# Performance work log

Measured on AMD Instinct MI355X. Metric: run time of the kernel, lower is better.

## Reference

```python
import jax, jax.numpy as jnp
import numpy as np

STRIDE = 32
NUM_CLASSES = 20
CONF_THRESH = 0.01
NMS_THRESH = 0.5
INPUT_H, INPUT_W = 1024, 1024
EPS = 1e-28


def make_grid(h, w):
    hs, ws = h // STRIDE, w // STRIDE
    gy, gx = jnp.meshgrid(jnp.arange(hs), jnp.arange(ws), indexing='ij')
    # [1, hs*ws, 2] (x, y) cell coordinates
    return jnp.stack([gx, gy], axis=-1).reshape(1, hs * ws, 2).astype(jnp.float32)


def decode_boxes(txtytwth, grid):
    # txtytwth: [B, N, 4] -> [xmin, ymin, xmax, ymax] in pixels
    cxy = (jax.nn.sigmoid(txtytwth[..., :2]) + grid) * STRIDE
    wh = jnp.exp(txtytwth[..., 2:])
    return jnp.concatenate([cxy - wh * 0.5, cxy + wh * 0.5], axis=-1)


def pairwise_iou(boxes):
    # boxes: [N, 4]; faithful to source: area without +1, w/h clamped to 1e-28
    x1, y1, x2, y2 = boxes[:, 0], boxes[:, 1], boxes[:, 2], boxes[:, 3]
    areas = (x2 - x1) * (y2 - y1)
    xx1 = jnp.maximum(x1[:, None], x1[None, :])
    yy1 = jnp.maximum(y1[:, None], y1[None, :])
    xx2 = jnp.minimum(x2[:, None], x2[None, :])
    yy2 = jnp.minimum(y2[:, None], y2[None, :])
    w = jnp.maximum(EPS, xx2 - xx1)
    h = jnp.maximum(EPS, yy2 - yy1)
    inter = w * h
    return inter / (areas[:, None] + areas[None, :] - inter)


def nms_single(boxes, scores, valid):
    # greedy NMS, fixed-shape: returns keep mask [N] in original order
    n = boxes.shape[0]
    order = jnp.argsort(-scores)
    b = boxes[order]
    v = valid[order]
    iou = pairwise_iou(b)  # [N, N]
    idx = jnp.arange(n)

    def body(i, keep):
        sup = keep[i] & (iou[i] > NMS_THRESH) & (idx > i)
        return keep & jnp.logical_not(sup)

    keep_sorted = jax.lax.fori_loop(0, n, body, v)
    return jnp.zeros(n, dtype=bool).at[order].set(keep_sorted)


def setup_inputs() -> dict:
    key = jax.random.key(0)
    k1, k2, k3 = jax.random.split(key, 3)
    feat = jax.random.normal(k1, (64, 512, 32, 32), dtype=jnp.float32)
    w_pred = jax.random.normal(k2, (25, 512), dtype=jnp.float32) * 0.05
    b_pred = jax.random.normal(k3, (25,), dtype=jnp.float32) * 0.05
    return {"feat": feat, "w_pred": w_pred, "b_pred": b_pred}


def reference(feat, w_pred, b_pred):
    B, C, hs, ws = feat.shape
    N = hs * ws
    # 1x1 conv head: [B, 25, hs, ws] -> [B, N, 25]
    pred = jnp.einsum('bchw,oc->bhwo', feat, w_pred) + b_pred
    pred = pred.reshape(B, N, 1 + NUM_CLASSES + 4)

    conf = jax.nn.sigmoid(pred[..., :1])                      # [B, N, 1]
    cls = jax.nn.softmax(pred[..., 1:1 + NUM_CLASSES], -1)    # [B, N, 20]
    boxes = decode_boxes(pred[..., 1 + NUM_CLASSES:], make_grid(INPUT_H, INPUT_W))
    scale = jnp.array([INPUT_W, INPUT_H, INPUT_W, INPUT_H], jnp.float32)
    boxes = jnp.clip(boxes / scale, 0.0, 1.0)                 # [B, N, 4] in [0,1]

    scores_all = conf * cls                                   # [B, N, 20]
    cls_inds = jnp.argmax(scores_all, axis=-1)                # [B, N]
    scores = jnp.max(scores_all, axis=-1)                     # [B, N]
    valid = scores > CONF_THRESH

    # class-aware NMS via per-class coordinate offset (boxes in [0,1])
    off_boxes = boxes + cls_inds[..., None].astype(jnp.float32) * 2.0
    keep = jax.vmap(nms_single)(off_boxes, scores, valid)     # [B, N] bool
    return boxes, scores, cls_inds.astype(jnp.int32), keep
```

## Files before the change

kernel.cpp:

```cpp
#include <hip/hip_runtime.h>
#include <hip/hip_bf16.h>

typedef unsigned long long u64;
typedef unsigned int u32;
typedef __attribute__((ext_vector_type(4))) double f64x4;

#define NB   64
#define NPOS 1024
#define NOUT 25
#define NCLS 20
#define ECAP_B 512
#define ECAP_S 2048
#define TINY_TH (30.0f / 1024.0f)

#define OFF_BIGC  0
#define OFF_BIGL  4096
#define OFF_EDGC  266240
#define OFF_EDGL  267264

__device__ __forceinline__ void epilogue(const double* __restrict__ acc,
                                         const float* __restrict__ bias,
                                         int b, int n, bool* isbig,
                                         float* __restrict__ boxes_out,
                                         float* __restrict__ scores_out,
                                         float* __restrict__ cls_out)
{
    double p[NOUT];
#pragma unroll
    for (int o = 0; o < NOUT; ++o) p[o] = acc[o] + (double)bias[o];

    double conf = 1.0 / (1.0 + exp(-p[0]));
    double m = p[1]; int ci = 0;
#pragma unroll
    for (int i = 2; i <= NCLS; ++i) {
        if (p[i] > m) { m = p[i]; ci = i - 1; }
    }
    double ssum = 0.0;
#pragma unroll
    for (int i = 0; i < NCLS; ++i) ssum += exp(p[1 + i] - m);
    double best = conf / ssum;

    int gx = n & 31, gy = n >> 5;
    double sx = 1.0 / (1.0 + exp(-p[21]));
    double sy = 1.0 / (1.0 + exp(-p[22]));
    double cx = (sx + (double)gx) * 32.0;
    double cy = (sy + (double)gy) * 32.0;
    double bw = exp(p[23]), bh = exp(p[24]);
    double x1 = (cx - bw * 0.5) * (1.0 / 1024.0);
    double y1 = (cy - bh * 0.5) * (1.0 / 1024.0);
    double x2 = (cx + bw * 0.5) * (1.0 / 1024.0);
    double y2 = (cy + bh * 0.5) * (1.0 / 1024.0);
    x1 = fmin(fmax(x1, 0.0), 1.0); y1 = fmin(fmax(y1, 0.0), 1.0);
    x2 = fmin(fmax(x2, 0.0), 1.0); y2 = fmin(fmax(y2, 0.0), 1.0);

    float fx1 = (float)x1, fy1 = (float)y1, fx2 = (float)x2, fy2 = (float)y2;
    int gi = b * NPOS + n;
    ((float4*)boxes_out)[gi] = make_float4(fx1, fy1, fx2, fy2);
    scores_out[gi] = (float)best;
    cls_out[gi]    = (float)ci;
    *isbig = !((fx2 - fx1 < TINY_TH) && (fy2 - fy1 < TINY_TH));
}

__global__ __launch_bounds__(256, 6) void k_main(const float* __restrict__ feat,
                                                 const float* __restrict__ w,
                                                 const float* __restrict__ bias,
                                                 float* __restrict__ boxes_out,
                                                 float* __restrict__ scores_out,
                                                 float* __restrict__ cls_out,
                                                 int* __restrict__ bigcntT,
                                                 int* __restrict__ biglistT)
{
    __shared__ __align__(16) char smem[24832];
    float* AbF = (float*)smem;
    float* BbF = (float*)(smem + 16384);
    double (*pd)[33] = (double(*)[33])smem;

    const int b   = blockIdx.y;
    const int tx  = blockIdx.x;
    const int tid = threadIdx.x;
    const int l   = tid & 63;
    const int wv  = tid >> 6;
    const int pg  = wv >> 1;
    const int oh  = wv & 1;
    const int n0  = tx * 64;

    double ca = ((l >> 4) == 0) ? (double)(l & 15) : 0.0;
    double cb = ((l >> 4) == 0) ? 1.0 : 0.0;
    f64x4 cd = {0.0, 0.0, 0.0, 0.0};
    cd = __builtin_amdgcn_mfma_f64_16x16x4f64(ca, cb, cd, 0, 0, 0);
    int rmap[4];
#pragma unroll
    for (int v = 0; v < 4; ++v) {
        int r = (int)(cd[v] + 0.5);
        rmap[v] = (r < 0) ? 0 : (r > 15 ? 15 : r);
    }

    const float* __restrict__ featb = feat + (size_t)b * 512 * NPOS + n0;
    const int bo = tid >> 5;
    const int bc = tid & 31;

#define A_SRC(C0, IT) (((const float4*)(featb + (size_t)((C0) + wv*8 + (IT)*4 + (l>>4)) * NPOS)) + (l & 15))
#define A_DST(BUF, IT) ((float4*)(AbF + (BUF)*2048 + (wv*8 + (IT)*4) * 64 + l*4))
#define B_LOAD(C0, P, DST) do {                                               \
    int o_ = (P)*8 + bo;                                                      \
    (DST) = (o_ < NOUT) ? w[(size_t)o_ * 512 + (C0) + bc] : 0.0f;             \
} while (0)
#define B_WRITE(BUF, P, V) (BbF[(BUF)*1056 + bc*33 + (P)*8 + bo] = (V))

    f64x4 acc0 = {0.0, 0.0, 0.0, 0.0};
    f64x4 acc1 = {0.0, 0.0, 0.0, 0.0};

    float4 ra0 = *A_SRC(0, 0), ra1 = *A_SRC(0, 1);
    float rb0, rb1, rb2, rb3;
    B_LOAD(0, 0, rb0); B_LOAD(0, 1, rb1); B_LOAD(0, 2, rb2); B_LOAD(0, 3, rb3);
    *A_DST(0, 0) = ra0;  *A_DST(0, 1) = ra1;
    B_WRITE(0, 0, rb0); B_WRITE(0, 1, rb1); B_WRITE(0, 2, rb2); B_WRITE(0, 3, rb3);
    __syncthreads();

#pragma unroll 1
    for (int t = 0; t < 16; ++t) {
        const int buf = t & 1;
        const bool more = (t + 1) < 16;
        const int c1 = (t + 1) * 32;
        if (more) {
            ra0 = *A_SRC(c1, 0);  ra1 = *A_SRC(c1, 1);
            B_LOAD(c1, 0, rb0); B_LOAD(c1, 1, rb1);
            B_LOAD(c1, 2, rb2); B_LOAD(c1, 3, rb3);
        }
#pragma unroll
        for (int s = 0; s < 8; ++s) {
            const int rowA = buf*2048 + (4*s + (l >> 4)) * 64 + pg * 32 + (l & 15);
            const int rowB = buf*1056 + (4*s + (l >> 4)) * 33 + oh * 16 + (l & 15);
            double av0 = (double)AbF[rowA];
            double av1 = (double)AbF[rowA + 16];
            double bv  = (double)BbF[rowB];
            acc0 = __builtin_amdgcn_mfma_f64_16x16x4f64(av0, bv, acc0, 0, 0, 0);
            acc1 = __builtin_amdgcn_mfma_f64_16x16x4f64(av1, bv, acc1, 0, 0, 0);
        }
        if (more) {
            *A_DST(buf ^ 1, 0) = ra0;  *A_DST(buf ^ 1, 1) = ra1;
            B_WRITE(buf ^ 1, 0, rb0); B_WRITE(buf ^ 1, 1, rb1);
            B_WRITE(buf ^ 1, 2, rb2); B_WRITE(buf ^ 1, 3, rb3);
        }
        __syncthreads();
    }
#undef A_SRC
#undef A_DST
#undef B_LOAD
#undef B_WRITE

#pragma unroll
    for (int v = 0; v < 4; ++v) {
        int r0 = pg * 32 + rmap[v];
        pd[r0][oh * 16 + (l & 15)]      = acc0[v];
        pd[r0 + 16][oh * 16 + (l & 15)] = acc1[v];
    }
    __syncthreads();

    if (tid < 64) {
        double acc[NOUT];
#pragma unroll
        for (int o = 0; o < NOUT; ++o) acc[o] = pd[tid][o];
        int n = n0 + tid;
        bool isbig;
        epilogue(acc, bias, b, n, &isbig, boxes_out, scores_out, cls_out);

        u64 mask = __ballot(isbig);
        if (isbig) {
            int slot = __popcll(mask & ((1ull << tid) - 1ull));
            biglistT[(b * 16 + tx) * 64 + slot] = n;
        }
        if (tid == 0) bigcntT[b * 16 + tx] = (int)__popcll(mask);
    }
}

__global__ __launch_bounds__(256) void k_edge(const float4* __restrict__ boxes4,
                                              const float* __restrict__ scores,
                                              const float* __restrict__ cls,
                                              const int* __restrict__ bigcntT,
                                              const int* __restrict__ biglistT,
                                              int* __restrict__ edgecntT,
                                              u32* __restrict__ edgesT)
{
    __shared__ int bl[NPOS];
    __shared__ int nbtot;
    __shared__ u32 eds[ECAP_B];
    __shared__ int ecnt;
    const int b  = blockIdx.y;
    const int bx = blockIdx.x;
    const int tid = threadIdx.x;
    const int p = bx * 256 + tid;

    if (tid == 0) {
        int s = 0;
        for (int t = 0; t < 16; ++t) {
            int c = bigcntT[b * 16 + t];
            for (int k = 0; k < c; ++k) bl[s++] = biglistT[(b * 16 + t) * 64 + k];
        }
        nbtot = s;
        ecnt = 0;
    }
    __syncthreads();

    const float sp = scores[b * NPOS + p];
    if (sp > 0.01f) {
        const float4 bp = boxes4[b * NPOS + p];
        const float ap = (bp.z - bp.x) * (bp.w - bp.y);
        const int cp = (int)cls[b * NPOS + p];
        const bool tinyp = (bp.z - bp.x < TINY_TH) && (bp.w - bp.y < TINY_TH);
        const int gx = p & 31, gy = p >> 5;

#define PAIR(I, NEEDTINY) do {                                                \
    int i_ = (I);                                                             \
    if (scores[b * NPOS + i_] > 0.01f) {                                      \
        float4 bi = boxes4[b * NPOS + i_];                                    \
        bool ok = true;                                                       \
        if (NEEDTINY)                                                         \
            ok = (bi.z - bi.x < TINY_TH) && (bi.w - bi.y < TINY_TH);          \
        if (ok && (int)cls[b * NPOS + i_] == cp) {                            \
            float xx1 = fmaxf(bi.x, bp.x), yy1 = fmaxf(bi.y, bp.y);           \
            float xx2 = fminf(bi.z, bp.z), yy2 = fminf(bi.w, bp.w);           \
            float ww = fmaxf(1e-28f, xx2 - xx1);                              \
            float hh = fmaxf(1e-28f, yy2 - yy1);                              \
            float inter = ww * hh;                                            \
            float ai = (bi.z - bi.x) * (bi.w - bi.y);                         \
            float uni = ai + ap - inter;                                      \
            if (uni > 0.0f && inter > 0.5f * uni) {                           \
                int u_ = p < i_ ? p : i_, v_ = p < i_ ? i_ : p;               \
                int slot = atomicAdd(&ecnt, 1);                               \
                if (slot < ECAP_B) eds[slot] = ((u32)u_ << 16) | (u32)v_;     \
            }                                                                 \
        }                                                                     \
    }                                                                         \
} while (0)

        if (tinyp) {
            if (gy > 0 && gx > 0)  PAIR(p - 33, true);
            if (gy > 0)            PAIR(p - 32, true);
            if (gy > 0 && gx < 31) PAIR(p - 31, true);
            if (gx > 0)            PAIR(p - 1,  true);
        }
        int nb = nbtot;
        for (int t = 0; t < nb; ++t) {
            int q = bl[t];
            if (q == p) continue;
            if (!tinyp && p > q) continue;
            PAIR(q, false);
        }
#undef PAIR
    }
    __syncthreads();

    int E = ecnt; if (E > ECAP_B) E = ECAP_B;
    if (tid == 0) edgecntT[b * 4 + bx] = E;
    for (int i = tid; i < E; i += 256)
        edgesT[(size_t)(b * 4 + bx) * ECAP_B + i] = eds[i];
}

__global__ __launch_bounds__(64) void k_resolve(const float* __restrict__ scores,
                                                const int* __restrict__ edgecntT,
                                                const u32* __restrict__ edgesT,
                                                float* __restrict__ keep_out)
{
    __shared__ u64 keepw[16];
    __shared__ u32 eds[ECAP_S];
    __shared__ u64 done[ECAP_S / 64];
    __shared__ int Esh;
    const int b = blockIdx.x, lane = threadIdx.x;

    for (int t = 0; t < 16; ++t) {
        bool v = scores[b * NPOS + t * 64 + lane] > 0.01f;
        u64 w = __ballot(v);
        if (lane == 0) keepw[t] = w;
    }
    if (lane < ECAP_S / 64) done[lane] = 0ull;
    if (lane == 0) {
        int off = 0;
        for (int e = 0; e < 4; ++e) {
            int c = edgecntT[b * 4 + e];
            if (c > ECAP_B) c = ECAP_B;
            for (int j = 0; j < c; ++j)
                eds[off++] = edgesT[(size_t)(b * 4 + e) * ECAP_B + j];
        }
        Esh = off;
    }
    __syncthreads();

    int E = Esh;
    if (lane == 0 && E > 0) {
        for (int it = 0; it < E; ++it) {
            int bestj = -1, bidx = 0, bsup = 0, btgt = 0;
            float bs = -1.0f;
            for (int j = 0; j < E; ++j) {
                if ((done[j >> 6] >> (j & 63)) & 1ull) continue;
                u32 e = eds[j];
                int u = (int)(e >> 16), v = (int)(e & 0xffffu);
                float su = scores[b * NPOS + u], sv = scores[b * NPOS + v];
                int sup, tgt; float ss;
                if (su > sv || (su == sv && u < v)) { sup = u; tgt = v; ss = su; }
                else                                { sup = v; tgt = u; ss = sv; }
                if (bestj < 0 || ss > bs || (ss == bs && sup < bidx)) {
                    bestj = j; bs = ss; bidx = sup; bsup = sup; btgt = tgt;
                }
            }
            done[bestj >> 6] |= 1ull << (bestj & 63);
            if ((keepw[bsup >> 6] >> (bsup & 63)) & 1ull)
                keepw[btgt >> 6] &= ~(1ull << (btgt & 63));
        }
    }
    __syncthreads();

    for (int t = 0; t < 16; ++t) {
        u64 w = keepw[t];
        keep_out[b * NPOS + t * 64 + lane] = ((w >> lane) & 1ull) ? 1.0f : 0.0f;
    }
}

extern "C" void kernel_launch(void* const* d_in, const int* in_sizes, int n_in,
                              void* d_out, int out_size, void* d_ws, size_t ws_size,
                              hipStream_t stream)
{
    const float* feat = (const float*)d_in[0];
    const float* w    = (const float*)d_in[1];
    const float* bias = (const float*)d_in[2];

    float* out = (float*)d_out;
    float* boxes_out  = out;
    float* scores_out = out + NB * NPOS * 4;
    float* cls_out    = out + NB * NPOS * 5;
    float* keep_out   = out + NB * NPOS * 6;

    char* ws = (char*)d_ws;
    int* bigcntT  = (int*)(ws + OFF_BIGC);
    int* biglistT = (int*)(ws + OFF_BIGL);
    int* edgecntT = (int*)(ws + OFF_EDGC);
    u32* edgesT   = (u32*)(ws + OFF_EDGL);

    hipLaunchKernelGGL(k_main,   dim3(16, 64), dim3(256), 0, stream, feat, w, bias,
                       boxes_out, scores_out, cls_out, bigcntT, biglistT);
    hipLaunchKernelGGL(k_edge,   dim3(4, 64),  dim3(256), 0, stream,
                       (const float4*)boxes_out, scores_out, cls_out,
                       bigcntT, biglistT, edgecntT, edgesT);
    hipLaunchKernelGGL(k_resolve, dim3(64),    dim3(64),  0, stream, scores_out,
                       edgecntT, edgesT, keep_out);
}
```

Before: 70.26 us.

## Fuse edge-building and NMS resolve kernels into one per-image kernel

Merges the edge-finding kernel (4 blocks per image) and the serial resolve kernel into a single block per image. Edges stay in shared memory instead of making a round trip through global workspace, and scores are cached in shared memory for both the pair tests and the resolve loop. This removes one launch and the global edge traffic, but runs the edge search with a quarter as many blocks, each thread looping over four positions. The total edge capacity also drops from 2048 to 1024.

```diff
diff --git a/kernel.cpp b/kernel.cpp
--- a/kernel.cpp
+++ b/kernel.cpp
@@ -9,14 +9,11 @@
 #define NPOS 1024
 #define NOUT 25
 #define NCLS 20
-#define ECAP_B 512
-#define ECAP_S 2048
+#define ECAP_S 1024
 #define TINY_TH (30.0f / 1024.0f)
 
 #define OFF_BIGC  0
 #define OFF_BIGL  4096
-#define OFF_EDGC  266240
-#define OFF_EDGL  267264
 
 __device__ __forceinline__ void epilogue(const double* __restrict__ acc,
                                          const float* __restrict__ bias,
@@ -174,22 +171,22 @@
     }
 }
 
-__global__ __launch_bounds__(256) void k_edge(const float4* __restrict__ boxes4,
-                                              const float* __restrict__ scores,
-                                              const float* __restrict__ cls,
-                                              const int* __restrict__ bigcntT,
-                                              const int* __restrict__ biglistT,
-                                              int* __restrict__ edgecntT,
-                                              u32* __restrict__ edgesT)
+__global__ __launch_bounds__(256) void k_nms(const float4* __restrict__ boxes4,
+                                             const float* __restrict__ scores,
+                                             const float* __restrict__ cls,
+                                             const int* __restrict__ bigcntT,
+                                             const int* __restrict__ biglistT,
+                                             float* __restrict__ keep_out)
 {
+    __shared__ float sc[NPOS];
     __shared__ int bl[NPOS];
     __shared__ int nbtot;
-    __shared__ u32 eds[ECAP_B];
+    __shared__ u32 eds[ECAP_S];
     __shared__ int ecnt;
-    const int b  = blockIdx.y;
-    const int bx = blockIdx.x;
-    const int tid = threadIdx.x;
-    const int p = bx * 256 + tid;
+    __shared__ u64 keepw[16];
+    __shared__ u64 done[ECAP_S / 64];
+    const int b = blockIdx.x, tid = threadIdx.x;
+    const int lane = tid & 63, w4 = tid >> 6;
 
     if (tid == 0) {
         int s = 0;
@@ -200,19 +197,31 @@
         nbtot = s;
         ecnt = 0;
     }
-    __syncthreads();
-
-    const float sp = scores[b * NPOS + p];
-    if (sp > 0.01f) {
-        const float4 bp = boxes4[b * NPOS + p];
-        const float ap = (bp.z - bp.x) * (bp.w - bp.y);
-        const int cp = (int)cls[b * NPOS + p];
-        const bool tinyp = (bp.z - bp.x < TINY_TH) && (bp.w - bp.y < TINY_TH);
-        const int gx = p & 31, gy = p >> 5;
+    if (tid < ECAP_S / 64) done[tid] = 0ull;
+#pragma unroll
+    for (int t = 0; t < 4; ++t) {
+        int word = w4 * 4 + t;
+        float s = scores[b * NPOS + word * 64 + lane];
+        sc[word * 64 + lane] = s;
+        u64 vb = __ballot(s > 0.01f);
+        if (lane == 0) keepw[word] = vb;
+    }
+    __syncthreads();
+
+    int nb = nbtot;
+#pragma unroll 1
+    for (int p = tid; p < NPOS; p += 256) {
+        float sp = sc[p];
+        if (sp <= 0.01f) continue;
+        float4 bp = boxes4[b * NPOS + p];
+        float ap = (bp.z - bp.x) * (bp.w - bp.y);
+        int cp = (int)cls[b * NPOS + p];
+        bool tinyp = (bp.z - bp.x < TINY_TH) && (bp.w - bp.y < TINY_TH);
+        int gx = p & 31, gy = p >> 5;
 
 #define PAIR(I, NEEDTINY) do {                                                \
     int i_ = (I);                                                             \
-    if (scores[b * NPOS + i_] > 0.01f) {                                      \
+    if (sc[i_] > 0.01f) {                                                     \
         float4 bi = boxes4[b * NPOS + i_];                                    \
         bool ok = true;                                                       \
         if (NEEDTINY)                                                         \
@@ -228,7 +237,7 @@
             if (uni > 0.0f && inter > 0.5f * uni) {                           \
                 int u_ = p < i_ ? p : i_, v_ = p < i_ ? i_ : p;               \
                 int slot = atomicAdd(&ecnt, 1);                               \
-                if (slot < ECAP_B) eds[slot] = ((u32)u_ << 16) | (u32)v_;     \
+                if (slot < ECAP_S) eds[slot] = ((u32)u_ << 16) | (u32)v_;     \
             }                                                                 \
         }                                                                     \
     }                                                                         \
@@ -240,9 +249,8 @@
             if (gy > 0 && gx < 31) PAIR(p - 31, true);
             if (gx > 0)            PAIR(p - 1,  true);
         }
-        int nb = nbtot;
-        for (int t = 0; t < nb; ++t) {
-            int q = bl[t];
+        for (int t2 = 0; t2 < nb; ++t2) {
+            int q = bl[t2];
             if (q == p) continue;
             if (!tinyp && p > q) continue;
             PAIR(q, false);
@@ -251,43 +259,8 @@
     }
     __syncthreads();
 
-    int E = ecnt; if (E > ECAP_B) E = ECAP_B;
-    if (tid == 0) edgecntT[b * 4 + bx] = E;
-    for (int i = tid; i < E; i += 256)
-        edgesT[(size_t)(b * 4 + bx) * ECAP_B + i] = eds[i];
-}
-
-__global__ __launch_bounds__(64) void k_resolve(const float* __restrict__ scores,
-                                                const int* __restrict__ edgecntT,
-                                                const u32* __restrict__ edgesT,
-                                                float* __restrict__ keep_out)
-{
-    __shared__ u64 keepw[16];
-    __shared__ u32 eds[ECAP_S];
-    __shared__ u64 done[ECAP_S / 64];
-    __shared__ int Esh;
-    const int b = blockIdx.x, lane = threadIdx.x;
-
-    for (int t = 0; t < 16; ++t) {
-        bool v = scores[b * NPOS + t * 64 + lane] > 0.01f;
-        u64 w = __ballot(v);
-        if (lane == 0) keepw[t] = w;
-    }
-    if (lane < ECAP_S / 64) done[lane] = 0ull;
-    if (lane == 0) {
-        int off = 0;
-        for (int e = 0; e < 4; ++e) {
-            int c = edgecntT[b * 4 + e];
-            if (c > ECAP_B) c = ECAP_B;
-            for (int j = 0; j < c; ++j)
-                eds[off++] = edgesT[(size_t)(b * 4 + e) * ECAP_B + j];
-        }
-        Esh = off;
-    }
-    __syncthreads();
-
-    int E = Esh;
-    if (lane == 0 && E > 0) {
+    if (tid == 0) {
+        int E = ecnt; if (E > ECAP_S) E = ECAP_S;
         for (int it = 0; it < E; ++it) {
             int bestj = -1, bidx = 0, bsup = 0, btgt = 0;
             float bs = -1.0f;
@@ -295,7 +268,7 @@
                 if ((done[j >> 6] >> (j & 63)) & 1ull) continue;
                 u32 e = eds[j];
                 int u = (int)(e >> 16), v = (int)(e & 0xffffu);
-                float su = scores[b * NPOS + u], sv = scores[b * NPOS + v];
+                float su = sc[u], sv = sc[v];
                 int sup, tgt; float ss;
                 if (su > sv || (su == sv && u < v)) { sup = u; tgt = v; ss = su; }
                 else                                { sup = v; tgt = u; ss = sv; }
@@ -310,9 +283,11 @@
     }
     __syncthreads();
 
-    for (int t = 0; t < 16; ++t) {
-        u64 w = keepw[t];
-        keep_out[b * NPOS + t * 64 + lane] = ((w >> lane) & 1ull) ? 1.0f : 0.0f;
+#pragma unroll
+    for (int t = 0; t < 4; ++t) {
+        int word = w4 * 4 + t;
+        u64 kw = keepw[word];
+        keep_out[b * NPOS + word * 64 + lane] = ((kw >> lane) & 1ull) ? 1.0f : 0.0f;
     }
 }
 
@@ -333,14 +308,10 @@
     char* ws = (char*)d_ws;
     int* bigcntT  = (int*)(ws + OFF_BIGC);
     int* biglistT = (int*)(ws + OFF_BIGL);
-    int* edgecntT = (int*)(ws + OFF_EDGC);
-    u32* edgesT   = (u32*)(ws + OFF_EDGL);
-
-    hipLaunchKernelGGL(k_main,   dim3(16, 64), dim3(256), 0, stream, feat, w, bias,
+
+    hipLaunchKernelGGL(k_main, dim3(16, 64), dim3(256), 0, stream, feat, w, bias,
                        boxes_out, scores_out, cls_out, bigcntT, biglistT);
-    hipLaunchKernelGGL(k_edge,   dim3(4, 64),  dim3(256), 0, stream,
+    hipLaunchKernelGGL(k_nms,  dim3(64),     dim3(256), 0, stream,
                        (const float4*)boxes_out, scores_out, cls_out,
-                       bigcntT, biglistT, edgecntT, edgesT);
-    hipLaunchKernelGGL(k_resolve, dim3(64),    dim3(64),  0, stream, scores_out,
-                       edgecntT, edgesT, keep_out);
+                       bigcntT, biglistT, keep_out);
 }
```

Measured after the change: 72.79 us. 1.04x slower.
